# Performance work log

Hardware: AMD Instinct MI355X
Metric: run time of the kernel (lower is better)

## Reference

```python
import jax, jax.numpy as jnp
import numpy as np

NUM_HEADS = 8
DIM = 384
KSIZE = 9  # res_kernel_size


def _moe_fc(x2d, gate_w, gate_b, w0, b0, w1, b1):
    # NaiveGate with top_k=1: softmax over a single top-1 logit == 1.0, so the
    # SparseDispatcher dispatch/exp/mul/log combine reduces exactly to selecting
    # the argmax expert's output per token.
    logits = x2d @ gate_w + gate_b                      # [T, 2]
    sel = jnp.argmax(logits, axis=-1)[:, None]          # [T, 1]
    y0 = x2d @ w0.T + b0
    y1 = x2d @ w1.T + b1
    return jnp.where(sel == 0, y0, y1)


def _forward(x, qkv_gate_w, qkv_gate_b, qkv_w0, qkv_w1,
             proj_gate_w, proj_gate_b, proj_w0, proj_b0, proj_w1, proj_b1,
             dconv_w):
    B, N, C = x.shape
    h, hd = NUM_HEADS, C // NUM_HEADS
    xt = x.reshape(-1, C)
    zero3 = jnp.zeros((3 * C,), x.dtype)  # qkv_bias=False
    qkv = _moe_fc(xt, qkv_gate_w, qkv_gate_b, qkv_w0, zero3, qkv_w1, zero3)
    qkv = qkv.reshape(B, N, 3, h, hd).transpose(2, 0, 3, 1, 4)  # [3,B,h,N,d]
    q, k, v = qkv[0], qkv[1], qkv[2]

    q = q / jnp.linalg.norm(q, axis=-1, keepdims=True)
    k = k / jnp.linalg.norm(k, axis=-1, keepdims=True)
    scale1 = jnp.mean(jnp.abs(q))
    scale2 = jnp.mean(jnp.abs(k))
    # straight-through binarization: fwd value = (x>0)*scale, grad flows via clamp(x,0,1)
    cq = jnp.clip(q, 0.0, 1.0)
    q = jax.lax.stop_gradient((q > 0).astype(q.dtype) * scale1 - cq) + cq
    ck = jnp.clip(k, 0.0, 1.0)
    k = jax.lax.stop_gradient((k > 0).astype(k.dtype) * scale2 - ck) + ck

    # depthwise residual conv over the token axis: v is [B, h, N, d], kernel (9,1)
    dconv_v = jax.lax.conv_general_dilated(
        v, dconv_w, window_strides=(1, 1), padding=[(KSIZE // 2, KSIZE // 2), (0, 0)],
        feature_group_count=h, dimension_numbers=("NCHW", "OIHW", "NCHW"))

    # linear-attention reorder: (K^T V) first -> O(N d^2)
    attn = jnp.einsum("bhnd,bhne->bhde", k, v)          # [B,h,d,d]
    out = 0.5 * v - (1.0 / jnp.pi) * jnp.einsum("bhnd,bhde->bhne", q, attn)
    out = out / jnp.linalg.norm(out, axis=-1, keepdims=True)
    out = out + dconv_v
    out = out.transpose(0, 2, 1, 3).reshape(B, N, C)

    out = _moe_fc(out.reshape(-1, C), proj_gate_w, proj_gate_b,
                  proj_w0, proj_b0, proj_w1, proj_b1)
    return out.reshape(B, N, C)


def setup_inputs() -> dict:
    key = jax.random.key(0)
    ks = jax.random.split(key, 12)
    B, N, C = 8, 4096, DIM
    s = 0.02
    return {
        "x": jax.random.normal(ks[0], (B, N, C), jnp.float32),
        "H": 64,
        "W": 64,
        "qkv_gate_w": jax.random.normal(ks[1], (C, 2), jnp.float32) * s,
        "qkv_gate_b": jnp.zeros((2,), jnp.float32),
        "qkv_w0": jax.random.normal(ks[2], (3 * C, C), jnp.float32) * s,
        "qkv_w1": jax.random.normal(ks[3], (3 * C, C), jnp.float32) * s,
        "proj_gate_w": jax.random.normal(ks[4], (C, 2), jnp.float32) * s,
        "proj_gate_b": jnp.zeros((2,), jnp.float32),
        "proj_w0": jax.random.normal(ks[5], (C, C), jnp.float32) * s,
        "proj_b0": jnp.zeros((C,), jnp.float32),
        "proj_w1": jax.random.normal(ks[6], (C, C), jnp.float32) * s,
        "proj_b1": jnp.zeros((C,), jnp.float32),
        "dconv_w": jax.random.normal(ks[7], (NUM_HEADS, 1, KSIZE, 1), jnp.float32) * s,
    }


def reference(x, H, W, qkv_gate_w, qkv_gate_b, qkv_w0, qkv_w1,
              proj_gate_w, proj_gate_b, proj_w0, proj_b0, proj_w1, proj_b1,
              dconv_w):
    # H, W are unused by the math (kept for signature fidelity)
    return _forward(x, qkv_gate_w, qkv_gate_b, qkv_w0, qkv_w1,
                    proj_gate_w, proj_gate_b, proj_w0, proj_b0, proj_w1, proj_b1,
                    dconv_w)
```

## Files before the change

kernel.cpp:

```cpp
#include <hip/hip_runtime.h>
#include <hip/hip_bf16.h>

#define BB 8
#define NN 4096
#define CC 384
#define HH 8
#define DD 48
#define TT (BB*NN)
#define CAP (TT + 128)
#define NQ ((size_t)BB*HH*NN*DD)
#define LISTCAP 32768

static_assert(CAP % 128 == 0, "cap");

typedef __attribute__((ext_vector_type(8))) short bf16x8;
typedef __attribute__((ext_vector_type(4))) float f32x4;

__device__ __forceinline__ float waveRedSum(float v){
  #pragma unroll
  for (int o = 32; o > 0; o >>= 1) v += __shfl_xor(v, o);
  return v;
}

__device__ __forceinline__ unsigned short f2bf(float f){
  unsigned u = __float_as_uint(f);
  u += 0x7FFFu + ((u >> 16) & 1u);
  return (unsigned short)(u >> 16);
}
__device__ __forceinline__ float bf2f(unsigned short h){
  return __uint_as_float(((unsigned)h) << 16);
}

__global__ void k_init(int* __restrict__ perm0, int* __restrict__ perm1, int* __restrict__ cur){
  int i = blockIdx.x * 256 + threadIdx.x;
  if (i < 8) cur[i] = 0;
  if (i < CAP){ perm0[i] = -1; perm1[i] = -1; }
}

__global__ void k_cvt_split(const float* __restrict__ src, unsigned short* __restrict__ hi,
                            unsigned short* __restrict__ lo, int n4){
  int i = blockIdx.x*256 + threadIdx.x;
  if (i >= n4) return;
  float4 v = ((const float4*)src)[i];
  float f[4] = {v.x, v.y, v.z, v.w};
  unsigned short h[4], l[4];
  #pragma unroll
  for (int j = 0; j < 4; j++){
    h[j] = f2bf(f[j]);
    l[j] = f2bf(f[j] - bf2f(h[j]));
  }
  uint2 hv, lv;
  hv.x = h[0] | ((unsigned)h[1] << 16); hv.y = h[2] | ((unsigned)h[3] << 16);
  lv.x = l[0] | ((unsigned)l[1] << 16); lv.y = l[2] | ((unsigned)l[3] << 16);
  ((uint2*)hi)[i] = hv;
  ((uint2*)lo)[i] = lv;
}

__global__ void k_gate_scatter(const float* __restrict__ X,
                               const float* __restrict__ gw, const float* __restrict__ gb,
                               int* __restrict__ perm, int* __restrict__ cur,
                               unsigned char* __restrict__ selb){
  const int lane = threadIdx.x & 63;
  const int wave = threadIdx.x >> 6;
  float gd[6];
  #pragma unroll
  for (int j = 0; j < 6; j++){
    int c = lane + 64*j;
    gd[j] = gw[c*2+1] - gw[c*2];
  }
  const float gbd = gb[1] - gb[0];
  const int tok0 = (blockIdx.x*4 + wave) * 32;
  unsigned mask = 0u;
  for (int i = 0; i < 32; i++){
    const float* xr = X + (size_t)(tok0 + i) * CC;
    float d = 0.f;
    #pragma unroll
    for (int j = 0; j < 6; j++) d = fmaf(xr[lane + 64*j], gd[j], d);
    d = waveRedSum(d);
    if (d + gbd > 0.f) mask |= (1u << i);
  }
  int n1 = __popc(mask), n0 = 32 - n1;
  int b0 = 0, b1 = 0;
  if (lane == 0){
    b0 = atomicAdd(cur + 0, n0);
    b1 = atomicAdd(cur + 1, n1);
  }
  b0 = __shfl(b0, 0); b1 = __shfl(b1, 0);
  if (lane < 32){
    int sel = (mask >> lane) & 1;
    unsigned below = mask & ((1u << lane) - 1u);
    int r1 = __popc(below);
    int r0 = lane - r1;
    int idx = sel ? (CAP - 1 - (b1 + r1)) : (b0 + r0);
    perm[idx] = tok0 + lane;
    selb[tok0 + lane] = (unsigned char)sel;
  }
}

__global__ void k_gate2(const float* __restrict__ gpart, const float* __restrict__ gb,
                        int* __restrict__ perm, int* __restrict__ cur){
  const int t = blockIdx.x*256 + threadIdx.x;
  const int lane = threadIdx.x & 63;
  const float gbd = gb[1] - gb[0];
  float4 a = ((const float4*)(gpart + (size_t)t*8))[0];
  float4 c = ((const float4*)(gpart + (size_t)t*8))[1];
  float d = ((a.x + a.y) + (a.z + a.w)) + ((c.x + c.y) + (c.z + c.w)) + gbd;
  bool sel = d > 0.f;
  unsigned long long m = __ballot(sel);
  int n1 = (int)__popcll(m);
  int b0 = 0, b1 = 0;
  if (lane == 0){
    b0 = atomicAdd(cur + 0, 64 - n1);
    b1 = atomicAdd(cur + 1, n1);
  }
  b0 = __shfl(b0, 0); b1 = __shfl(b1, 0);
  unsigned long long below = m & ((1ull << lane) - 1ull);
  int r1 = (int)__popcll(below);
  int r0 = lane - r1;
  int idx = sel ? (CAP - 1 - (b1 + r1)) : (b0 + r0);
  perm[idx] = t;
}

template<int NCOLS, int PASSES, bool IS_QKV>
__global__ __launch_bounds__(256, 2)
void k_gemm_mfma(const unsigned short* __restrict__ Ahi_g, const unsigned short* __restrict__ Alo_g,
                 const unsigned short* __restrict__ W0h, const unsigned short* __restrict__ W0l,
                 const unsigned short* __restrict__ W1h, const unsigned short* __restrict__ W1l,
                 const float* __restrict__ bias0, const float* __restrict__ bias1,
                 const int* __restrict__ perm, const int* __restrict__ cur,
                 unsigned short* __restrict__ oq, unsigned short* __restrict__ ok,
                 float* __restrict__ ov, float* __restrict__ oproj,
                 int* __restrict__ tlist, int* __restrict__ tcnt)
{
  constexpr int GDX = NCOLS / 128;
  constexpr int NWG = GDX * (CAP/128);
  constexpr int NB = (PASSES == 3) ? 2 : 1;
  __shared__ unsigned short As[NB][128*32];
  __shared__ unsigned short Bs[NB][128*32];
  __shared__ int permv[128];

  int orig = blockIdx.y * GDX + blockIdx.x;
  constexpr int qq = NWG >> 3, rr = NWG & 7;
  int xcd = orig & 7, slot = orig >> 3;
  int logical = (xcd < rr) ? (xcd*(qq+1) + slot) : (rr*(qq+1) + (xcd-rr)*qq + slot);
  const int bx = logical % GDX, by = logical / GDX;

  const int tid = threadIdx.x;
  const int m0 = by * 128, n0 = bx * 128;
  if (tid < 128) permv[tid] = perm[m0 + tid];
  __syncthreads();
  const int expert = (m0 > cur[0]) ? 1 : 0;
  const unsigned short* Wh = expert ? W1h : W0h;
  const unsigned short* Wl = expert ? W1l : W0l;

  const int c0 = tid, c1 = tid + 256;
  const int r0 = c0 >> 2, r1 = c1 >> 2;
  const int s0 = (((c0 & 3) ^ ((r0 >> 1) & 3))) * 8;
  const int s1 = (((c1 & 3) ^ ((r1 >> 1) & 3))) * 8;
  int t0 = permv[r0]; if (t0 < 0) t0 = 0;
  int t1 = permv[r1]; if (t1 < 0) t1 = 0;
  const unsigned short* a0h = Ahi_g + (size_t)t0*CC + s0;
  const unsigned short* a1h = Ahi_g + (size_t)t1*CC + s1;
  const unsigned short* b0h = Wh + (size_t)(n0 + r0)*CC + s0;
  const unsigned short* b1h = Wh + (size_t)(n0 + r1)*CC + s1;
  const unsigned short* a0l = nullptr; const unsigned short* a1l = nullptr;
  const unsigned short* b0l = nullptr; const unsigned short* b1l = nullptr;
  if constexpr (PASSES == 3){
    a0l = Alo_g + (size_t)t0*CC + s0;
    a1l = Alo_g + (size_t)t1*CC + s1;
    b0l = Wl + (size_t)(n0 + r0)*CC + s0;
    b1l = Wl + (size_t)(n0 + r1)*CC + s1;
  }
  const int d0 = c0*8, d1 = c1*8;

  const int lane = tid & 63;
  const int wv = tid >> 6, wr = wv >> 1, wc2 = wv & 1;
  const int lr = lane & 15, lg = lane >> 4;

  f32x4 acc[4][4];
  #pragma unroll
  for (int i = 0; i < 4; i++)
    #pragma unroll
    for (int j = 0; j < 4; j++) acc[i][j] = (f32x4){0.f, 0.f, 0.f, 0.f};

  int aoff[4], boff[4];
  #pragma unroll
  for (int f = 0; f < 4; f++){
    int ra = wr*64 + f*16 + lr;
    aoff[f] = ra*32 + ((lg ^ ((ra >> 1) & 3)) * 8);
    int rb = wc2*64 + f*16 + lr;
    boff[f] = rb*32 + ((lg ^ ((rb >> 1) & 3)) * 8);
  }

  #define GLD(gp, lp) __builtin_amdgcn_global_load_lds( \
      (const __attribute__((address_space(1))) void*)(gp), \
      (__attribute__((address_space(3))) void*)(lp), 16, 0, 0)

  for (int ko = 0; ko < CC; ko += 32){
    GLD(a0h + ko, &As[0][d0]);
    GLD(a1h + ko, &As[0][d1]);
    GLD(b0h + ko, &Bs[0][d0]);
    GLD(b1h + ko, &Bs[0][d1]);
    if constexpr (PASSES == 3){
      GLD(a0l + ko, &As[1][d0]);
      GLD(a1l + ko, &As[1][d1]);
      GLD(b0l + ko, &Bs[1][d0]);
      GLD(b1l + ko, &Bs[1][d1]);
    }
    __syncthreads();
    bf16x8 ah[4], bh[4], al[4], bl[4];
    #pragma unroll
    for (int f = 0; f < 4; f++){
      ah[f] = *(const bf16x8*)&As[0][aoff[f]];
      bh[f] = *(const bf16x8*)&Bs[0][boff[f]];
      if constexpr (PASSES == 3){
        al[f] = *(const bf16x8*)&As[1][aoff[f]];
        bl[f] = *(const bf16x8*)&Bs[1][boff[f]];
      }
    }
    #pragma unroll
    for (int mf = 0; mf < 4; mf++)
      #pragma unroll
      for (int nf = 0; nf < 4; nf++){
        acc[mf][nf] = __builtin_amdgcn_mfma_f32_16x16x32_bf16(ah[mf], bh[nf], acc[mf][nf], 0, 0, 0);
        if constexpr (PASSES == 3){
          acc[mf][nf] = __builtin_amdgcn_mfma_f32_16x16x32_bf16(al[mf], bh[nf], acc[mf][nf], 0, 0, 0);
          acc[mf][nf] = __builtin_amdgcn_mfma_f32_16x16x32_bf16(ah[mf], bl[nf], acc[mf][nf], 0, 0, 0);
        }
      }
    __syncthreads();
  }
  #undef GLD

  #pragma unroll
  for (int mf = 0; mf < 4; mf++){
    #pragma unroll
    for (int j = 0; j < 4; j++){
      const int rl = wr*64 + mf*16 + lg*4 + j;
      const int t = permv[rl];
      if (t < 0) continue;
      const int b = t >> 12, nn = t & 4095;
      #pragma unroll
      for (int nf = 0; nf < 4; nf++){
        const int col = n0 + wc2*64 + nf*16 + lr;
        const float val = acc[mf][nf][j];
        if constexpr (IS_QKV){
          const int which = col / CC;
          const int rem = col - which*CC;
          const int h = rem / DD;
          const int e = rem - h*DD;
          const size_t off = (((size_t)b*HH + h)*NN + nn)*DD + e;
          if (which == 0){
            oq[off] = f2bf(val);
            if (fabsf(val) < 2.5e-5f){
              int pq = atomicAdd(tcnt, 1);
              if (pq < LISTCAP) tlist[pq] = (int)off;
            }
          } else if (which == 1){
            ok[off] = f2bf(val);
            if (fabsf(val) < 2.5e-5f){
              int pq = atomicAdd(tcnt, 1);
              if (pq < LISTCAP) tlist[pq] = (int)(off + NQ);
            }
          } else {
            ov[off] = val;
          }
        } else {
          const float* bs = expert ? bias1 : bias0;
          oproj[(size_t)t*CC + col] = val + bs[col];
        }
      }
    }
  }
}

__global__ void k_topup_fix(unsigned short* __restrict__ qb, unsigned short* __restrict__ kb,
                            const int* __restrict__ list, const int* __restrict__ cnt,
                            const float* __restrict__ x,
                            const float* __restrict__ w0, const float* __restrict__ w1,
                            const unsigned char* __restrict__ selb){
  const int lane = threadIdx.x & 63;
  const int gw = (blockIdx.x*256 + threadIdx.x) >> 6;
  const int nwaves = gridDim.x * 4;
  int n = cnt[0]; if (n > LISTCAP) n = LISTCAP;
  for (int e = gw; e < n; e += nwaves){
    int idx = list[e];
    int isK = (idx >= (int)NQ);
    int li = isK ? idx - (int)NQ : idx;
    int d = li % DD; int rest = li / DD;
    int nn = rest & 4095; int bh = rest >> 12;
    int b = bh >> 3, h = bh & 7;
    int t = b*NN + nn;
    int col = (isK ? CC : 0) + h*DD + d;
    const float* w = selb[t] ? w1 : w0;
    const float* xr = x + (size_t)t*CC;
    const float* wr = w + (size_t)col*CC;
    float s = 0.f;
    #pragma unroll
    for (int j = 0; j < 6; j++) s = fmaf(xr[lane + 64*j], wr[lane + 64*j], s);
    s = waveRedSum(s);
    if (lane == 0) (isK ? kb : qb)[li] = f2bf(s);
  }
}

__global__ void k_scales(const unsigned short* __restrict__ qb, const unsigned short* __restrict__ kb,
                         float* __restrict__ part){
  __shared__ float sq[256], sk[256];
  const int row = blockIdx.x*256 + threadIdx.x;
  const uint4* qp = (const uint4*)(qb + (size_t)row*DD);
  const uint4* kp = (const uint4*)(kb + (size_t)row*DD);
  float qss = 0.f, qsa = 0.f, kss = 0.f, ksa = 0.f;
  #pragma unroll
  for (int j = 0; j < 6; j++){
    uint4 u = qp[j];
    unsigned w[4] = {u.x, u.y, u.z, u.w};
    #pragma unroll
    for (int q2 = 0; q2 < 4; q2++){
      float f0 = bf2f((unsigned short)(w[q2] & 0xFFFFu));
      float f1 = bf2f((unsigned short)(w[q2] >> 16));
      qss = fmaf(f0, f0, qss); qsa += fabsf(f0);
      qss = fmaf(f1, f1, qss); qsa += fabsf(f1);
    }
    uint4 v = kp[j];
    unsigned w2[4] = {v.x, v.y, v.z, v.w};
    #pragma unroll
    for (int q2 = 0; q2 < 4; q2++){
      float f0 = bf2f((unsigned short)(w2[q2] & 0xFFFFu));
      float f1 = bf2f((unsigned short)(w2[q2] >> 16));
      kss = fmaf(f0, f0, kss); ksa += fabsf(f0);
      kss = fmaf(f1, f1, kss); ksa += fabsf(f1);
    }
  }
  sq[threadIdx.x] = qsa / sqrtf(qss);
  sk[threadIdx.x] = ksa / sqrtf(kss);
  __syncthreads();
  for (int s = 128; s > 0; s >>= 1){
    if (threadIdx.x < s){ sq[threadIdx.x] += sq[threadIdx.x+s]; sk[threadIdx.x] += sk[threadIdx.x+s]; }
    __syncthreads();
  }
  if (threadIdx.x == 0){
    part[blockIdx.x*2+0] = sq[0];
    part[blockIdx.x*2+1] = sk[0];
  }
}

__global__ void k_scales_reduce(const float* __restrict__ part, float* __restrict__ scalesb){
  __shared__ float sq[256], sk[256];
  const int t = threadIdx.x;
  float aq = 0.f, ak = 0.f;
  for (int i = t; i < 1024; i += 256){ aq += part[2*i]; ak += part[2*i+1]; }
  sq[t] = aq; sk[t] = ak;
  __syncthreads();
  for (int s = 128; s > 0; s >>= 1){
    if (t < s){ sq[t] += sq[t+s]; sk[t] += sk[t+s]; }
    __syncthreads();
  }
  if (t == 0){
    scalesb[0] = sq[0] * (1.0f/12582912.0f);
    scalesb[1] = sk[0] * (1.0f/12582912.0f);
  }
}

__global__ void k_attn_partial(const unsigned short* __restrict__ kb, const float* __restrict__ vb,
                               float* __restrict__ part){
  __shared__ float ks[64][48];
  __shared__ float vs[64][48];
  const int bh = blockIdx.x, seg = blockIdx.y;
  const int tid = threadIdx.x;
  const int ti = tid >> 5;
  const int tj = (tid >> 2) & 7;
  const int sl = tid & 3;
  const int dd0 = ti*6, ee0 = tj*6;
  const unsigned short* kbase = kb + ((size_t)bh*NN + seg*512) * DD;
  const float* vbase = vb + ((size_t)bh*NN + seg*512) * DD;
  float acc[6][6] = {};
  for (int c = 0; c < 8; c++){
    __syncthreads();
    for (int f = tid*2; f < 3072; f += 512){
      unsigned kk2 = *(const unsigned*)(kbase + c*3072 + f);
      float2 vv2 = *(const float2*)(vbase + c*3072 + f);
      (&ks[0][0])[f]   = ((short)(unsigned short)(kk2 & 0xFFFFu) > 0) ? 1.f : 0.f;
      (&ks[0][0])[f+1] = ((short)(unsigned short)(kk2 >> 16) > 0) ? 1.f : 0.f;
      (&vs[0][0])[f]   = vv2.x;
      (&vs[0][0])[f+1] = vv2.y;
    }
    __syncthreads();
    for (int nl = sl*16; nl < sl*16 + 16; nl++){
      float kk[6], vv[6];
      #pragma unroll
      for (int i = 0; i < 6; i++){ kk[i] = ks[nl][dd0+i]; vv[i] = vs[nl][ee0+i]; }
      #pragma unroll
      for (int i = 0; i < 6; i++)
        #pragma unroll
        for (int j = 0; j < 6; j++)
          acc[i][j] = fmaf(kk[i], vv[j], acc[i][j]);
    }
  }
  float* p = part + ((size_t)seg*64 + bh) * (DD*DD);
  #pragma unroll
  for (int i = 0; i < 6; i++)
    #pragma unroll
    for (int j = 0; j < 6; j++){
      float a = acc[i][j];
      a += __shfl_xor(a, 1);
      a += __shfl_xor(a, 2);
      if (sl == 0) p[(dd0+i)*48 + (ee0+j)] = a;
    }
}

__global__ void k_attn_reduce(const float* __restrict__ part, const float* __restrict__ scalesb,
                              unsigned short* __restrict__ aTh, unsigned short* __restrict__ aTl){
  const int bh = blockIdx.x;
  const float s2 = scalesb[1];
  for (int f = threadIdx.x; f < 3072; f += 256){
    const int e = f >> 6, d = f & 63;
    float s = 0.f;
    if (d < 48){
      #pragma unroll
      for (int seg = 0; seg < 8; seg++) s += part[((size_t)seg*64 + bh)*2304 + d*48 + e];
      s *= s2;
    }
    unsigned short hi = f2bf(s);
    aTh[(size_t)bh*3072 + f] = hi;
    aTl[(size_t)bh*3072 + f] = f2bf(s - bf2f(hi));
  }
}

__global__ __launch_bounds__(256, 4)
void k_fused(const unsigned short* __restrict__ qb, const float* __restrict__ vb,
             const unsigned short* __restrict__ aTh, const unsigned short* __restrict__ aTl,
             const float* __restrict__ scalesb, const float* __restrict__ dw,
             const float* __restrict__ pgw,
             unsigned short* __restrict__ intermh, float* __restrict__ gpart){
  __shared__ unsigned short aT[2][48*72];
  __shared__ float S_lds[128*48];
  __shared__ float wc[16];
  const int chunk = blockIdx.x;
  const int bh = blockIdx.y;
  const int b = bh >> 3, h = bh & 7;
  const int tid = threadIdx.x;
  const int lane = tid & 63, w = tid >> 6;
  const int lr = lane & 15, lg = lane >> 4;

  for (int idx = tid; idx < 384; idx += 256){
    const int e = idx >> 3, sl = idx & 7;
    *(uint4*)&aT[0][e*72 + sl*8] = *(const uint4*)(aTh + (size_t)bh*3072 + e*64 + sl*8);
    *(uint4*)&aT[1][e*72 + sl*8] = *(const uint4*)(aTl + (size_t)bh*3072 + e*64 + sl*8);
  }
  if (tid < 9) wc[tid] = dw[h*9 + tid];
  __syncthreads();

  bf16x8 afr[2][2];
  #pragma unroll
  for (int m = 0; m < 2; m++){
    #pragma unroll
    for (int ks = 0; ks < 2; ks++){
      const int d0 = ks*32 + lg*8;
      bf16x8 a = (bf16x8){0,0,0,0,0,0,0,0};
      if (d0 < 48){
        const int tok = chunk*128 + (w*2+m)*16 + lr;
        uint4 raw = *(const uint4*)(qb + ((size_t)bh*NN + tok)*DD + d0);
        unsigned wd[4] = {raw.x, raw.y, raw.z, raw.w};
        #pragma unroll
        for (int i2 = 0; i2 < 8; i2++){
          unsigned short el = (unsigned short)((wd[i2 >> 1] >> ((i2 & 1)*16)) & 0xFFFFu);
          a[i2] = ((short)el > 0) ? (short)0x3F80 : (short)0;
        }
      }
      afr[m][ks] = a;
    }
  }
  f32x4 acc[2][3];
  #pragma unroll
  for (int m = 0; m < 2; m++)
    #pragma unroll
    for (int nf = 0; nf < 3; nf++) acc[m][nf] = (f32x4){0.f,0.f,0.f,0.f};
  #pragma unroll
  for (int nf = 0; nf < 3; nf++){
    bf16x8 bhv[2], blv[2];
    #pragma unroll
    for (int ks = 0; ks < 2; ks++){
      const int bo = (nf*16 + lr)*72 + ks*32 + lg*8;
      bhv[ks] = *(const bf16x8*)&aT[0][bo];
      blv[ks] = *(const bf16x8*)&aT[1][bo];
    }
    #pragma unroll
    for (int m = 0; m < 2; m++)
      #pragma unroll
      for (int ks = 0; ks < 2; ks++){
        acc[m][nf] = __builtin_amdgcn_mfma_f32_16x16x32_bf16(afr[m][ks], bhv[ks], acc[m][nf], 0, 0, 0);
        acc[m][nf] = __builtin_amdgcn_mfma_f32_16x16x32_bf16(afr[m][ks], blv[ks], acc[m][nf], 0, 0, 0);
      }
  }
  #pragma unroll
  for (int m = 0; m < 2; m++)
    #pragma unroll
    for (int nf = 0; nf < 3; nf++)
      #pragma unroll
      for (int j = 0; j < 4; j++)
        S_lds[((w*2+m)*16 + lg*4 + j)*48 + nf*16 + lr] = acc[m][nf][j];
  __syncthreads();

  const float coef = scalesb[0] * 0.31830988618379067f;
  const float gdh = (lane < 48) ? (pgw[(h*48+lane)*2+1] - pgw[(h*48+lane)*2]) : 0.f;
  const float* vrow = vb + (size_t)bh*NN*DD;
  const int n0 = chunk*128 + w*32;
  float ring[9];
  #pragma unroll
  for (int k2 = 0; k2 < 8; k2++){
    int nn2 = n0 - 4 + k2;
    ring[k2] = (nn2 >= 0 && nn2 < NN && lane < 48) ? vrow[(size_t)nn2*DD + lane] : 0.f;
  }
  for (int it = 0; it < 32; it++){
    const int n = n0 + it;
    const int nh = n + 4;
    ring[8] = (nh < NN && lane < 48) ? vrow[(size_t)nh*DD + lane] : 0.f;
    const float vv = ring[4];
    const float Sv = (lane < 48) ? S_lds[(w*32 + it)*48 + lane] : 0.f;
    float op = 0.5f*vv - coef*Sv;
    float ss = waveRedSum(op*op);
    float res = op / sqrtf(ss);
    float dc = 0.f;
    #pragma unroll
    for (int k2 = 0; k2 < 9; k2++) dc = fmaf(wc[k2], ring[k2], dc);
    float r = res + dc;
    if (lane < 48)
      intermh[((size_t)b*NN + n)*CC + h*DD + lane] = f2bf(r);
    float gp = waveRedSum(r*gdh);
    if (lane == 0) gpart[((size_t)b*NN + n)*8 + h] = gp;
    #pragma unroll
    for (int k2 = 0; k2 < 8; k2++) ring[k2] = ring[k2+1];
  }
}

extern "C" void kernel_launch(void* const* d_in, const int* in_sizes, int n_in,
                              void* d_out, int out_size, void* d_ws, size_t ws_size,
                              hipStream_t stream){
  const float* x    = (const float*)d_in[0];
  const float* qgw  = (const float*)d_in[3];
  const float* qgb  = (const float*)d_in[4];
  const float* qw0  = (const float*)d_in[5];
  const float* qw1  = (const float*)d_in[6];
  const float* pgw  = (const float*)d_in[7];
  const float* pgb  = (const float*)d_in[8];
  const float* pw0  = (const float*)d_in[9];
  const float* pb0  = (const float*)d_in[10];
  const float* pw1  = (const float*)d_in[11];
  const float* pb1  = (const float*)d_in[12];
  const float* dw   = (const float*)d_in[13];
  float* out = (float*)d_out;

  char* p = (char*)d_ws;
  auto alloc = [&](size_t bytes){ char* r = p; p += (bytes + 255) & ~(size_t)255; return r; };

  unsigned short* qbuf = (unsigned short*)alloc(2*NQ);
  unsigned short* kbuf = (unsigned short*)alloc(2*NQ);
  float* vbuf          = (float*)alloc(4*NQ);
  char* xreg           = alloc(4*NQ);
  unsigned short* Xhi  = (unsigned short*)xreg;
  unsigned short* Xlo  = Xhi + NQ;
  unsigned short* intermh = (unsigned short*)xreg;
  unsigned short* qw0h = (unsigned short*)alloc(2*1152*384);
  unsigned short* qw0l = (unsigned short*)alloc(2*1152*384);
  unsigned short* qw1h = (unsigned short*)alloc(2*1152*384);
  unsigned short* qw1l = (unsigned short*)alloc(2*1152*384);
  unsigned short* pw0h = (unsigned short*)alloc(2*384*384);
  unsigned short* pw0l = (unsigned short*)alloc(2*384*384);
  unsigned short* pw1h = (unsigned short*)alloc(2*384*384);
  unsigned short* pw1l = (unsigned short*)alloc(2*384*384);
  float* attn_part     = (float*)alloc(4*(size_t)8*64*2304);
  unsigned short* aTh  = (unsigned short*)alloc(2*(size_t)64*3072);
  unsigned short* aTl  = (unsigned short*)alloc(2*(size_t)64*3072);
  float* scale_part    = (float*)alloc(4*2048);
  float* scalesb       = (float*)alloc(64);
  float* gpart         = (float*)alloc(4*(size_t)TT*8);
  int* perm_qkv        = (int*)alloc(4*CAP);
  int* perm_proj       = (int*)alloc(4*CAP);
  int* cur             = (int*)alloc(64);
  int* list            = (int*)alloc(4*LISTCAP);
  unsigned char* selq  = (unsigned char*)alloc(TT);

  k_init<<<(CAP + 255)/256, 256, 0, stream>>>(perm_qkv, perm_proj, cur);

  k_cvt_split<<<(int)(NQ/4 + 255)/256, 256, 0, stream>>>(x, Xhi, Xlo, (int)(NQ/4));
  k_cvt_split<<<(1152*384/4 + 255)/256, 256, 0, stream>>>(qw0, qw0h, qw0l, 1152*384/4);
  k_cvt_split<<<(1152*384/4 + 255)/256, 256, 0, stream>>>(qw1, qw1h, qw1l, 1152*384/4);
  k_cvt_split<<<(384*384/4 + 255)/256, 256, 0, stream>>>(pw0, pw0h, pw0l, 384*384/4);
  k_cvt_split<<<(384*384/4 + 255)/256, 256, 0, stream>>>(pw1, pw1h, pw1l, 384*384/4);

  k_gate_scatter<<<256, 256, 0, stream>>>(x, qgw, qgb, perm_qkv, cur, selq);

  {
    dim3 g(9, CAP/128);
    k_gemm_mfma<1152, 3, true><<<g, 256, 0, stream>>>(
        Xhi, Xlo, qw0h, qw0l, qw1h, qw1l, nullptr, nullptr,
        perm_qkv, cur, qbuf, kbuf, vbuf, nullptr, list, cur + 4);
  }

  k_topup_fix<<<64, 256, 0, stream>>>(qbuf, kbuf, list, cur + 4, x, qw0, qw1, selq);

  k_scales<<<1024, 256, 0, stream>>>(qbuf, kbuf, scale_part);
  k_scales_reduce<<<1, 256, 0, stream>>>(scale_part, scalesb);

  {
    dim3 g(64, 8);
    k_attn_partial<<<g, 256, 0, stream>>>(kbuf, vbuf, attn_part);
  }
  k_attn_reduce<<<64, 256, 0, stream>>>(attn_part, scalesb, aTh, aTl);

  {
    dim3 g(32, 64);
    k_fused<<<g, 256, 0, stream>>>(qbuf, vbuf, aTh, aTl, scalesb, dw, pgw, intermh, gpart);
  }

  k_gate2<<<TT/256, 256, 0, stream>>>(gpart, pgb, perm_proj, cur + 2);

  {
    dim3 g(3, CAP/128);
    k_gemm_mfma<384, 1, false><<<g, 256, 0, stream>>>(
        intermh, nullptr, pw0h, pw0l, pw1h, pw1l, pb0, pb1,
        perm_proj, cur + 2, nullptr, nullptr, nullptr, out, nullptr, nullptr);
  }
}
```

Before: 378.5 us.

## Double-buffer GEMM LDS tiles, merge weight conversions, fold scale reduction, widen gate grid

The MFMA GEMM now double-buffers its LDS tiles, prefetching the next k-slice while the current one is computed, and drops one barrier per iteration. The four weight-conversion launches become a single kernel. The single-block scale reduction is folded into the attention-reduce kernel, with every block recomputing it redundantly. The gate scatter uses 8 tokens per wave across 1024 blocks instead of 32 tokens per wave across 256 blocks, which adds parallelism but quadruples the atomics. Doubling LDS for the 3-pass GEMM to 64KB may limit occupancy under launch_bounds(256,2).

```diff
diff --git a/kernel.cpp b/kernel.cpp
--- a/kernel.cpp
+++ b/kernel.cpp
@@ -56,6 +56,35 @@
   ((uint2*)lo)[i] = lv;
 }
 
+__global__ void k_cvt_weights(const float* __restrict__ qw0, const float* __restrict__ qw1,
+                              const float* __restrict__ pw0, const float* __restrict__ pw1,
+                              unsigned short* __restrict__ qw0h, unsigned short* __restrict__ qw0l,
+                              unsigned short* __restrict__ qw1h, unsigned short* __restrict__ qw1l,
+                              unsigned short* __restrict__ pw0h, unsigned short* __restrict__ pw0l,
+                              unsigned short* __restrict__ pw1h, unsigned short* __restrict__ pw1l){
+  const int NQW = 1152*384/4, NPW = 384*384/4;
+  int i = blockIdx.x*256 + threadIdx.x;
+  const float* src; unsigned short* hi; unsigned short* lo; int off;
+  if (i < NQW){ src = qw0; hi = qw0h; lo = qw0l; off = i; }
+  else if (i < 2*NQW){ src = qw1; hi = qw1h; lo = qw1l; off = i - NQW; }
+  else if (i < 2*NQW + NPW){ src = pw0; hi = pw0h; lo = pw0l; off = i - 2*NQW; }
+  else if (i < 2*NQW + 2*NPW){ src = pw1; hi = pw1h; lo = pw1l; off = i - 2*NQW - NPW; }
+  else return;
+  float4 v = ((const float4*)src)[off];
+  float f[4] = {v.x, v.y, v.z, v.w};
+  unsigned short h[4], l[4];
+  #pragma unroll
+  for (int j = 0; j < 4; j++){
+    h[j] = f2bf(f[j]);
+    l[j] = f2bf(f[j] - bf2f(h[j]));
+  }
+  uint2 hv, lv;
+  hv.x = h[0] | ((unsigned)h[1] << 16); hv.y = h[2] | ((unsigned)h[3] << 16);
+  lv.x = l[0] | ((unsigned)l[1] << 16); lv.y = l[2] | ((unsigned)l[3] << 16);
+  ((uint2*)hi)[off] = hv;
+  ((uint2*)lo)[off] = lv;
+}
+
 __global__ void k_gate_scatter(const float* __restrict__ X,
                                const float* __restrict__ gw, const float* __restrict__ gb,
                                int* __restrict__ perm, int* __restrict__ cur,
@@ -69,9 +98,9 @@
     gd[j] = gw[c*2+1] - gw[c*2];
   }
   const float gbd = gb[1] - gb[0];
-  const int tok0 = (blockIdx.x*4 + wave) * 32;
+  const int tok0 = (blockIdx.x*4 + wave) * 8;
   unsigned mask = 0u;
-  for (int i = 0; i < 32; i++){
+  for (int i = 0; i < 8; i++){
     const float* xr = X + (size_t)(tok0 + i) * CC;
     float d = 0.f;
     #pragma unroll
@@ -79,14 +108,14 @@
     d = waveRedSum(d);
     if (d + gbd > 0.f) mask |= (1u << i);
   }
-  int n1 = __popc(mask), n0 = 32 - n1;
+  int n1 = __popc(mask), n0 = 8 - n1;
   int b0 = 0, b1 = 0;
   if (lane == 0){
     b0 = atomicAdd(cur + 0, n0);
     b1 = atomicAdd(cur + 1, n1);
   }
   b0 = __shfl(b0, 0); b1 = __shfl(b1, 0);
-  if (lane < 32){
+  if (lane < 8){
     int sel = (mask >> lane) & 1;
     unsigned below = mask & ((1u << lane) - 1u);
     int r1 = __popc(below);
@@ -135,8 +164,8 @@
   constexpr int GDX = NCOLS / 128;
   constexpr int NWG = GDX * (CAP/128);
   constexpr int NB = (PASSES == 3) ? 2 : 1;
-  __shared__ unsigned short As[NB][128*32];
-  __shared__ unsigned short Bs[NB][128*32];
+  __shared__ unsigned short As[2][NB][128*32];
+  __shared__ unsigned short Bs[2][NB][128*32];
   __shared__ int permv[128];
 
   int orig = blockIdx.y * GDX + blockIdx.x;
@@ -196,26 +225,32 @@
       (const __attribute__((address_space(1))) void*)(gp), \
       (__attribute__((address_space(3))) void*)(lp), 16, 0, 0)
 
+  #define STAGE(bi, KO) do { \
+    GLD(a0h + (KO), &As[bi][0][d0]); \
+    GLD(a1h + (KO), &As[bi][0][d1]); \
+    GLD(b0h + (KO), &Bs[bi][0][d0]); \
+    GLD(b1h + (KO), &Bs[bi][0][d1]); \
+    if constexpr (PASSES == 3){ \
+      GLD(a0l + (KO), &As[bi][1][d0]); \
+      GLD(a1l + (KO), &As[bi][1][d1]); \
+      GLD(b0l + (KO), &Bs[bi][1][d0]); \
+      GLD(b1l + (KO), &Bs[bi][1][d1]); \
+    } \
+  } while(0)
+
+  STAGE(0, 0);
+  __syncthreads();
   for (int ko = 0; ko < CC; ko += 32){
-    GLD(a0h + ko, &As[0][d0]);
-    GLD(a1h + ko, &As[0][d1]);
-    GLD(b0h + ko, &Bs[0][d0]);
-    GLD(b1h + ko, &Bs[0][d1]);
-    if constexpr (PASSES == 3){
-      GLD(a0l + ko, &As[1][d0]);
-      GLD(a1l + ko, &As[1][d1]);
-      GLD(b0l + ko, &Bs[1][d0]);
-      GLD(b1l + ko, &Bs[1][d1]);
-    }
-    __syncthreads();
+    const int cb = (ko >> 5) & 1;
+    if (ko + 32 < CC) STAGE(cb ^ 1, ko + 32);
     bf16x8 ah[4], bh[4], al[4], bl[4];
     #pragma unroll
     for (int f = 0; f < 4; f++){
-      ah[f] = *(const bf16x8*)&As[0][aoff[f]];
-      bh[f] = *(const bf16x8*)&Bs[0][boff[f]];
+      ah[f] = *(const bf16x8*)&As[cb][0][aoff[f]];
+      bh[f] = *(const bf16x8*)&Bs[cb][0][boff[f]];
       if constexpr (PASSES == 3){
-        al[f] = *(const bf16x8*)&As[1][aoff[f]];
-        bl[f] = *(const bf16x8*)&Bs[1][boff[f]];
+        al[f] = *(const bf16x8*)&As[cb][1][aoff[f]];
+        bl[f] = *(const bf16x8*)&Bs[cb][1][boff[f]];
       }
     }
     #pragma unroll
@@ -230,6 +265,7 @@
       }
     __syncthreads();
   }
+  #undef STAGE
   #undef GLD
 
   #pragma unroll
@@ -344,23 +380,6 @@
   }
 }
 
-__global__ void k_scales_reduce(const float* __restrict__ part, float* __restrict__ scalesb){
-  __shared__ float sq[256], sk[256];
-  const int t = threadIdx.x;
-  float aq = 0.f, ak = 0.f;
-  for (int i = t; i < 1024; i += 256){ aq += part[2*i]; ak += part[2*i+1]; }
-  sq[t] = aq; sk[t] = ak;
-  __syncthreads();
-  for (int s = 128; s > 0; s >>= 1){
-    if (t < s){ sq[t] += sq[t+s]; sk[t] += sk[t+s]; }
-    __syncthreads();
-  }
-  if (t == 0){
-    scalesb[0] = sq[0] * (1.0f/12582912.0f);
-    scalesb[1] = sk[0] * (1.0f/12582912.0f);
-  }
-}
-
 __global__ void k_attn_partial(const unsigned short* __restrict__ kb, const float* __restrict__ vb,
                                float* __restrict__ part){
   __shared__ float ks[64][48];
@@ -408,11 +427,26 @@
     }
 }
 
-__global__ void k_attn_reduce(const float* __restrict__ part, const float* __restrict__ scalesb,
-                              unsigned short* __restrict__ aTh, unsigned short* __restrict__ aTl){
+__global__ void k_attn_reduce(const float* __restrict__ part, const float* __restrict__ scale_part,
+                              unsigned short* __restrict__ aTh, unsigned short* __restrict__ aTl,
+                              float* __restrict__ scalesb){
+  __shared__ float sq[256], sk[256];
+  const int t = threadIdx.x;
+  float aq = 0.f, ak = 0.f;
+  for (int i = t; i < 1024; i += 256){ aq += scale_part[2*i]; ak += scale_part[2*i+1]; }
+  sq[t] = aq; sk[t] = ak;
+  __syncthreads();
+  for (int s = 128; s > 0; s >>= 1){
+    if (t < s){ sq[t] += sq[t+s]; sk[t] += sk[t+s]; }
+    __syncthreads();
+  }
+  const float s2 = sk[0] * (1.0f/12582912.0f);
+  if (blockIdx.x == 0 && t == 0){
+    scalesb[0] = sq[0] * (1.0f/12582912.0f);
+    scalesb[1] = s2;
+  }
   const int bh = blockIdx.x;
-  const float s2 = scalesb[1];
-  for (int f = threadIdx.x; f < 3072; f += 256){
+  for (int f = t; f < 3072; f += 256){
     const int e = f >> 6, d = f & 63;
     float s = 0.f;
     if (d < 48){
@@ -583,12 +617,11 @@
   k_init<<<(CAP + 255)/256, 256, 0, stream>>>(perm_qkv, perm_proj, cur);
 
   k_cvt_split<<<(int)(NQ/4 + 255)/256, 256, 0, stream>>>(x, Xhi, Xlo, (int)(NQ/4));
-  k_cvt_split<<<(1152*384/4 + 255)/256, 256, 0, stream>>>(qw0, qw0h, qw0l, 1152*384/4);
-  k_cvt_split<<<(1152*384/4 + 255)/256, 256, 0, stream>>>(qw1, qw1h, qw1l, 1152*384/4);
-  k_cvt_split<<<(384*384/4 + 255)/256, 256, 0, stream>>>(pw0, pw0h, pw0l, 384*384/4);
-  k_cvt_split<<<(384*384/4 + 255)/256, 256, 0, stream>>>(pw1, pw1h, pw1l, 384*384/4);
-
-  k_gate_scatter<<<256, 256, 0, stream>>>(x, qgw, qgb, perm_qkv, cur, selq);
+  k_cvt_weights<<<1152, 256, 0, stream>>>(qw0, qw1, pw0, pw1,
+                                          qw0h, qw0l, qw1h, qw1l,
+                                          pw0h, pw0l, pw1h, pw1l);
+
+  k_gate_scatter<<<1024, 256, 0, stream>>>(x, qgw, qgb, perm_qkv, cur, selq);
 
   {
     dim3 g(9, CAP/128);
@@ -600,13 +633,12 @@
   k_topup_fix<<<64, 256, 0, stream>>>(qbuf, kbuf, list, cur + 4, x, qw0, qw1, selq);
 
   k_scales<<<1024, 256, 0, stream>>>(qbuf, kbuf, scale_part);
-  k_scales_reduce<<<1, 256, 0, stream>>>(scale_part, scalesb);
 
   {
     dim3 g(64, 8);
     k_attn_partial<<<g, 256, 0, stream>>>(kbuf, vbuf, attn_part);
   }
-  k_attn_reduce<<<64, 256, 0, stream>>>(attn_part, scalesb, aTh, aTl);
+  k_attn_reduce<<<64, 256, 0, stream>>>(attn_part, scale_part, aTh, aTl, scalesb);
 
   {
     dim3 g(32, 64);
```

New measurement: 449.7 us. 18.8% more time.
